# Kernel optimization log

Measured on AMD Instinct MI355X. Metric: run time of the kernel, lower is better.

Reference implementation:

```python
import jax, jax.numpy as jnp
import numpy as np

B, T, C, H = 2, 2048, 1024, 16
HD = C // H
HID = C * 4 // 3  # 1365, SwiGLU hidden
EPS = 1e-5


def _ln(x, g, b):
    m = x.mean(-1, keepdims=True)
    v = ((x - m) ** 2).mean(-1, keepdims=True)
    return (x - m) / jnp.sqrt(v + EPS) * g + b


def setup_inputs() -> dict:
    key0 = jax.random.key(0)
    ks = jax.random.split(key0, 16)
    s = 0.02
    inp = {
        'query': jax.random.normal(ks[0], (B, T, C), jnp.float32),
        'key': jax.random.normal(ks[1], (B, T, C), jnp.float32),
        'g_q': jnp.ones((C,), jnp.float32), 'b_q': jnp.zeros((C,), jnp.float32),
        'g_k': jnp.ones((C,), jnp.float32), 'b_k': jnp.zeros((C,), jnp.float32),
        'in_proj_w': jax.random.normal(ks[2], (3 * C, C), jnp.float32) * s,
        'in_proj_b': jnp.zeros((3 * C,), jnp.float32),
        'out_w': jax.random.normal(ks[3], (C, C), jnp.float32) * s,
        'out_b': jnp.zeros((C,), jnp.float32),
        'proj_w': jax.random.normal(ks[4], (C, C), jnp.float32) * s,
        'proj_b': jnp.zeros((C,), jnp.float32),
        'rel_table': jax.random.normal(ks[5], (H, 2 * 2048 - 1), jnp.float32) * s,
        'g_ffn': jnp.ones((C,), jnp.float32), 'b_ffn': jnp.zeros((C,), jnp.float32),
        'w1': jax.random.normal(ks[6], (HID, C), jnp.float32) * s,
        'w2': jax.random.normal(ks[7], (HID, C), jnp.float32) * s,
        'w3': jax.random.normal(ks[8], (C, HID), jnp.float32) * s,
        'g_out': jnp.ones((C,), jnp.float32), 'b_out': jnp.zeros((C,), jnp.float32),
        'max_len': 2048,
    }
    return inp


def reference(query, key, g_q, b_q, g_k, b_k, in_proj_w, in_proj_b, out_w, out_b,
              proj_w, proj_b, rel_table, g_ffn, b_ffn, w1, w2, w3, g_out, b_out, max_len):
    Tq, Tk = query.shape[1], key.shape[1]
    q = _ln(query, g_q, b_q)
    k = _ln(key, g_k, b_k)
    # in-projection (torch MHA packed weights)
    wq, wk, wv = jnp.split(in_proj_w, 3, axis=0)
    bq, bk, bv = jnp.split(in_proj_b, 3, axis=0)
    qp = (q @ wq.T + bq).reshape(B, Tq, H, HD).transpose(0, 2, 1, 3)
    kp = (k @ wk.T + bk).reshape(B, Tk, H, HD).transpose(0, 2, 1, 3)
    vp = (k @ wv.T + bv).reshape(B, Tk, H, HD).transpose(0, 2, 1, 3)
    # relative-position bias, mean over heads -> [Tq,Tk] additive mask
    rel_idx = jnp.clip(jnp.arange(Tq)[:, None] - jnp.arange(Tk)[None, :] + (max_len - 1),
                       0, 2 * max_len - 2)
    mask = rel_table[:, rel_idx].mean(axis=0)  # [Tq,Tk]
    scores = jnp.einsum('bhqd,bhkd->bhqk', qp, kp) / jnp.sqrt(jnp.float32(HD))
    attn = jax.nn.softmax(scores + mask[None, None], axis=-1)
    ctx = jnp.einsum('bhqk,bhkd->bhqd', attn, vp)
    ctx = ctx.transpose(0, 2, 1, 3).reshape(B, Tq, C)
    attn_out = ctx @ out_w.T + out_b
    attn_out = attn_out @ proj_w.T + proj_b
    x = query + attn_out
    # SwiGLU FFN (proj dropout/dropout are identity at eval)
    h = _ln(x, g_ffn, b_ffn)
    ff = (jax.nn.silu(h @ w1.T) * (h @ w2.T)) @ w3.T
    x = x + ff
    return _ln(x, g_out, b_out)
```

## Files before the change

kernel.cpp:

```cpp
#include <hip/hip_runtime.h>
#include <hip/hip_bf16.h>

static constexpr int Bb  = 2;
static constexpr int Tt  = 2048;
static constexpr int Cc  = 1024;
static constexpr int Hh  = 16;
static constexpr int HDi = 64;
static constexpr int HID = 1365;
static constexpr int HIDP = 1408;
static constexpr int Mm  = Bb * Tt;

typedef unsigned short u16;
typedef __attribute__((ext_vector_type(8))) short bf16x8;
typedef __attribute__((ext_vector_type(4))) float f32x4;
typedef __attribute__((ext_vector_type(8))) unsigned short u16x8;
typedef __attribute__((ext_vector_type(4))) unsigned short u16x4;

__device__ inline u16 f2bf(float f) {
    unsigned u = __builtin_bit_cast(unsigned, f);
    u += 0x7fffu + ((u >> 16) & 1u);
    return (u16)(u >> 16);
}

__device__ inline unsigned cvtpk(float lo, float hi) {
    unsigned r;
    asm("v_cvt_pk_bf16_f32 %0, %1, %2" : "=v"(r) : "v"(lo), "v"(hi));
    return r;
}

__device__ inline float vexp2(float x) {
    float r;
    asm("v_exp_f32 %0, %1" : "=v"(r) : "v"(x));
    return r;
}

__device__ inline void gl16(const void* g, void* l) {
    __builtin_amdgcn_global_load_lds(
        (const __attribute__((address_space(1))) unsigned*)g,
        (__attribute__((address_space(3))) unsigned*)l, 16, 0, 0);
}

template<int OUTBF>
__global__ __launch_bounds__(256) void ln_k(const float* __restrict__ x,
                                            const float* __restrict__ g,
                                            const float* __restrict__ b,
                                            void* __restrict__ yv) {
    int row = blockIdx.x;
    int tid = threadIdx.x;
    const float4* xr = (const float4*)(x + (size_t)row * Cc);
    float4 v = xr[tid];
    float s  = v.x + v.y + v.z + v.w;
    float ss = v.x*v.x + v.y*v.y + v.z*v.z + v.w*v.w;
    __shared__ float rs[256], rq[256];
    rs[tid] = s; rq[tid] = ss;
    __syncthreads();
    for (int o = 128; o > 0; o >>= 1) {
        if (tid < o) { rs[tid] += rs[tid+o]; rq[tid] += rq[tid+o]; }
        __syncthreads();
    }
    float mean = rs[0] * (1.f/Cc);
    float var  = rq[0] * (1.f/Cc) - mean*mean;
    float inv  = rsqrtf(var + 1e-5f);
    float4 gv = ((const float4*)g)[tid];
    float4 bv = ((const float4*)b)[tid];
    float o0 = (v.x-mean)*inv*gv.x + bv.x;
    float o1 = (v.y-mean)*inv*gv.y + bv.y;
    float o2 = (v.z-mean)*inv*gv.z + bv.z;
    float o3 = (v.w-mean)*inv*gv.w + bv.w;
    if (OUTBF) {
        u16x4 o4 = { f2bf(o0), f2bf(o1), f2bf(o2), f2bf(o3) };
        ((u16x4*)((u16*)yv + (size_t)row * Cc))[tid] = o4;
    } else {
        float4 o4 = { o0, o1, o2, o3 };
        ((float4*)((float*)yv + (size_t)row * Cc))[tid] = o4;
    }
}

__global__ __launch_bounds__(256) void ln2_k(const float* __restrict__ q,
                                             const float* __restrict__ k,
                                             const float* __restrict__ gq, const float* __restrict__ bq,
                                             const float* __restrict__ gk, const float* __restrict__ bk,
                                             u16* __restrict__ qn, u16* __restrict__ kn) {
    int row = blockIdx.x;
    const float* x; const float* g; const float* bb; u16* y; int r;
    if (row < Mm) { x = q; g = gq; bb = bq; y = qn; r = row; }
    else          { x = k; g = gk; bb = bk; y = kn; r = row - Mm; }
    int tid = threadIdx.x;
    float4 v = ((const float4*)(x + (size_t)r * Cc))[tid];
    float s  = v.x + v.y + v.z + v.w;
    float ss = v.x*v.x + v.y*v.y + v.z*v.z + v.w*v.w;
    __shared__ float rs[256], rq2[256];
    rs[tid] = s; rq2[tid] = ss;
    __syncthreads();
    for (int o = 128; o > 0; o >>= 1) {
        if (tid < o) { rs[tid] += rs[tid+o]; rq2[tid] += rq2[tid+o]; }
        __syncthreads();
    }
    float mean = rs[0] * (1.f/Cc);
    float var  = rq2[0] * (1.f/Cc) - mean*mean;
    float inv  = rsqrtf(var + 1e-5f);
    float4 gv = ((const float4*)g)[tid];
    float4 bv = ((const float4*)bb)[tid];
    u16x4 o4 = { f2bf((v.x-mean)*inv*gv.x + bv.x), f2bf((v.y-mean)*inv*gv.y + bv.y),
                 f2bf((v.z-mean)*inv*gv.z + bv.z), f2bf((v.w-mean)*inv*gv.w + bv.w) };
    ((u16x4*)(y + (size_t)r * Cc))[tid] = o4;
}

__global__ __launch_bounds__(256) void prep_k(const float* __restrict__ in_proj_w, u16* __restrict__ wA,
                                              const float* __restrict__ proj_w,  u16* __restrict__ wPb,
                                              const float* __restrict__ w1, u16* __restrict__ w1b,
                                              const float* __restrict__ w2, u16* __restrict__ w2b,
                                              const float* __restrict__ w3, u16* __restrict__ w3b,
                                              const float* __restrict__ out_w, u16* __restrict__ wOt,
                                              const float* __restrict__ out_b, const float* __restrict__ bp,
                                              float* __restrict__ bc,
                                              const float* __restrict__ rel, float* __restrict__ mr) {
    __shared__ float sh[64*65];
    int bid = blockIdx.x, tid = threadIdx.x;
    if (bid < 3456) {
        int u = bid * 256 + tid;
        const float* src; u16* dst; int valid;
        if (u < 1536*256)                   { src = in_proj_w; dst = wA;  valid = 3*Cc*Cc; }
        else if ((u -= 1536*256) < 512*256) { src = proj_w;    dst = wPb; valid = Cc*Cc; }
        else if ((u -= 512*256) < 704*256)  { src = w1;        dst = w1b; valid = HID*Cc; }
        else     { u -= 704*256;              src = w2;        dst = w2b; valid = HID*Cc; }
        int e0 = u * 8;
        u16x8 o;
        if (e0 + 8 <= valid) {
            float4 a = *(const float4*)(src + e0);
            float4 b = *(const float4*)(src + e0 + 4);
            o[0]=f2bf(a.x); o[1]=f2bf(a.y); o[2]=f2bf(a.z); o[3]=f2bf(a.w);
            o[4]=f2bf(b.x); o[5]=f2bf(b.y); o[6]=f2bf(b.z); o[7]=f2bf(b.w);
        } else {
            #pragma unroll
            for (int j = 0; j < 8; j++) { int e = e0 + j; o[j] = f2bf(e < valid ? src[e] : 0.f); }
        }
        *(u16x8*)(dst + (size_t)e0) = o;
    } else if (bid < 4160) {
        int idx = (bid - 3456) * 256 + tid;
        int e0 = idx * 8;
        int r = e0 / HIDP, c0 = e0 - r * HIDP;
        u16x8 o;
        #pragma unroll
        for (int j = 0; j < 8; j++) {
            int c = c0 + j;
            o[j] = f2bf(c < HID ? w3[(size_t)r * HID + c] : 0.f);
        }
        *(u16x8*)(w3b + (size_t)e0) = o;
    } else if (bid < 4416) {
        int id = bid - 4160;
        int j0 = (id & 15) * 64, c0 = (id >> 4) * 64;
        #pragma unroll
        for (int i = 0; i < 16; i++) {
            int e = tid + i*256;
            int c = e >> 6, j = e & 63;
            sh[c*65 + j] = out_w[(size_t)(c0 + c) * Cc + j0 + j];
        }
        __syncthreads();
        #pragma unroll
        for (int i = 0; i < 16; i++) {
            int e = tid + i*256;
            int j = e >> 6, c = e & 63;
            wOt[(size_t)(j0 + j) * Cc + c0 + c] = f2bf(sh[c*65 + j]);
        }
    } else if (bid < 5440) {
        int i = bid - 4416;
        float4 w = ((const float4*)(proj_w + (size_t)i * Cc))[tid];
        float4 b = ((const float4*)out_b)[tid];
        float s = w.x*b.x + w.y*b.y + w.z*b.z + w.w*b.w;
        sh[tid] = s; __syncthreads();
        for (int o = 128; o > 0; o >>= 1) {
            if (tid < o) sh[tid] += sh[tid+o];
            __syncthreads();
        }
        if (tid == 0) bc[i] = sh[0] + bp[i];
    } else {
        int j = (bid - 5440) * 256 + tid;
        if (j < 2*Tt - 1) {
            float s = 0.f;
            #pragma unroll
            for (int h = 0; h < Hh; h++) s += rel[(size_t)h * (2*Tt - 1) + j];
            mr[j] = s * (1.f/Hh);
        }
    }
}

template<int OUTBF, int HASRES, int HASBIAS>
__global__ __launch_bounds__(256) void mgemm64_k(const u16* __restrict__ A,
                                                 const u16* __restrict__ W,
                                                 const float* __restrict__ bias,
                                                 const float* __restrict__ res,
                                                 void* __restrict__ outv,
                                                 int N, int K) {
    __shared__ u16 As[2][64*32];
    __shared__ u16 Ws[2][128*32];
    int bm = blockIdx.y * 64, bn = blockIdx.x * 128;
    int tid = threadIdx.x, w = tid >> 6, l = tid & 63;
    int lr = l & 15, lh = l >> 4;
    int wm = (w >> 1) * 32, wn = (w & 1) * 64;
    f32x4 acc[2][4] = {};

    auto stage = [&](int buf, int kt) {
        {
            int row = tid >> 2, slot = tid & 3;
            int ko = kt + ((slot ^ (row & 3)) << 3);
            gl16(A + (size_t)(bm + row) * K + ko, (char*)As[buf] + tid * 16);
        }
        #pragma unroll
        for (int c = 0; c < 2; c++) {
            int i = c*256 + tid;
            int row = i >> 2, slot = i & 3;
            int ko = kt + ((slot ^ (row & 3)) << 3);
            gl16(W + (size_t)(bn + row) * K + ko, (char*)Ws[buf] + (c*256 + tid) * 16);
        }
    };
    stage(0, 0);
    for (int kt = 0; kt < K; kt += 32) {
        int buf = (kt >> 5) & 1;
        __syncthreads();
        if (kt + 32 < K) stage(buf ^ 1, kt + 32);
        bf16x8 af[2], wf[4];
        #pragma unroll
        for (int f = 0; f < 2; f++) {
            int r = wm + f*16 + lr;
            af[f] = *(const bf16x8*)((const char*)As[buf] + r*64 + ((lh ^ (r & 3)) << 4));
        }
        #pragma unroll
        for (int f = 0; f < 4; f++) {
            int rn = wn + f*16 + lr;
            wf[f] = *(const bf16x8*)((const char*)Ws[buf] + rn*64 + ((lh ^ (rn & 3)) << 4));
        }
        #pragma unroll
        for (int fm = 0; fm < 2; fm++)
            #pragma unroll
            for (int fn = 0; fn < 4; fn++)
                acc[fm][fn] = __builtin_amdgcn_mfma_f32_16x16x32_bf16(af[fm], wf[fn], acc[fm][fn], 0, 0, 0);
    }

    #pragma unroll
    for (int fm = 0; fm < 2; fm++) {
        #pragma unroll
        for (int r = 0; r < 4; r++) {
            int row = bm + wm + fm*16 + lh*4 + r;
            #pragma unroll
            for (int fn = 0; fn < 4; fn++) {
                int col = bn + wn + fn*16 + lr;
                float v = acc[fm][fn][r];
                if (HASBIAS) v += bias[col];
                if (HASRES)  v += res[(size_t)row * N + col];
                if (OUTBF) ((u16*)outv)[(size_t)row * N + col] = f2bf(v);
                else       ((float*)outv)[(size_t)row * N + col] = v;
            }
        }
    }
}

__global__ __launch_bounds__(256) void mqkv_k(const u16* __restrict__ qn,
                                              const u16* __restrict__ kn,
                                              const u16* __restrict__ wA,
                                              const float* __restrict__ bias3,
                                              u16* __restrict__ out3,
                                              const u16* __restrict__ wPb,
                                              const u16* __restrict__ wOt,
                                              u16* __restrict__ wCb) {
    int z = blockIdx.z;
    const u16* A; const u16* W; const float* bias = bias3; u16* out;
    if (z < 3) { A = z ? kn : qn; W = wA + (size_t)z * Cc * Cc; bias = bias3 + z * Cc; out = out3 + (size_t)z * Mm * Cc; }
    else       { if (blockIdx.y >= 8) return; A = wPb; W = wOt; out = wCb; }

    __shared__ u16 As[2][128*32];
    __shared__ u16 Ws[2][128*32];
    int bm = blockIdx.y * 128, bn = blockIdx.x * 128;
    int tid = threadIdx.x, w = tid >> 6, l = tid & 63;
    int lr = l & 15, lh = l >> 4;
    int wm = (w >> 1) * 64, wn = (w & 1) * 64;
    f32x4 acc[4][4] = {};

    auto stage = [&](int buf, int kt) {
        #pragma unroll
        for (int c = 0; c < 2; c++) {
            int i = w*128 + c*64 + l;
            int row = i >> 2, slot = i & 3;
            int ko = kt + ((slot ^ (row & 3)) << 3);
            gl16(A + (size_t)(bm + row) * Cc + ko, (char*)As[buf] + (w*128 + c*64) * 16);
            gl16(W + (size_t)(bn + row) * Cc + ko, (char*)Ws[buf] + (w*128 + c*64) * 16);
        }
    };
    stage(0, 0);
    for (int kt = 0; kt < Cc; kt += 32) {
        int buf = (kt >> 5) & 1;
        __syncthreads();
        if (kt + 32 < Cc) stage(buf ^ 1, kt + 32);
        bf16x8 af[4], wf[4];
        #pragma unroll
        for (int f = 0; f < 4; f++) {
            int r = wm + f*16 + lr;
            af[f] = *(const bf16x8*)((const char*)As[buf] + r*64 + ((lh ^ (r & 3)) << 4));
            int rn = wn + f*16 + lr;
            wf[f] = *(const bf16x8*)((const char*)Ws[buf] + rn*64 + ((lh ^ (rn & 3)) << 4));
        }
        #pragma unroll
        for (int fm = 0; fm < 4; fm++)
            #pragma unroll
            for (int fn = 0; fn < 4; fn++)
                acc[fm][fn] = __builtin_amdgcn_mfma_f32_16x16x32_bf16(af[fm], wf[fn], acc[fm][fn], 0, 0, 0);
    }

    #pragma unroll
    for (int fm = 0; fm < 4; fm++) {
        #pragma unroll
        for (int r = 0; r < 4; r++) {
            int row = bm + wm + fm*16 + lh*4 + r;
            #pragma unroll
            for (int fn = 0; fn < 4; fn++) {
                int col = bn + wn + fn*16 + lr;
                float v = acc[fm][fn][r];
                if (z < 3) v += bias[col];
                out[(size_t)row * Cc + col] = f2bf(v);
            }
        }
    }
}

__global__ __launch_bounds__(256) void mswiglu64_k(const u16* __restrict__ A,
                                                   const u16* __restrict__ W1,
                                                   const u16* __restrict__ W2,
                                                   u16* __restrict__ out,
                                                   int N, int K) {
    __shared__ u16 As[2][64*32];
    __shared__ u16 W1s[2][128*32];
    __shared__ u16 W2s[2][128*32];
    int bm = blockIdx.y * 64, bn = blockIdx.x * 128;
    int tid = threadIdx.x, w = tid >> 6, l = tid & 63;
    int lr = l & 15, lh = l >> 4;
    int wm = (w >> 1) * 32, wn = (w & 1) * 64;
    f32x4 acc1[2][4] = {};
    f32x4 acc2[2][4] = {};

    auto stage = [&](int buf, int kt) {
        {
            int row = tid >> 2, slot = tid & 3;
            int ko = kt + ((slot ^ (row & 3)) << 3);
            gl16(A + (size_t)(bm + row) * K + ko, (char*)As[buf] + tid * 16);
        }
        #pragma unroll
        for (int c = 0; c < 2; c++) {
            int i = c*256 + tid;
            int row = i >> 2, slot = i & 3;
            int ko = kt + ((slot ^ (row & 3)) << 3);
            gl16(W1 + (size_t)(bn + row) * K + ko, (char*)W1s[buf] + (c*256 + tid) * 16);
            gl16(W2 + (size_t)(bn + row) * K + ko, (char*)W2s[buf] + (c*256 + tid) * 16);
        }
    };
    stage(0, 0);
    for (int kt = 0; kt < K; kt += 32) {
        int buf = (kt >> 5) & 1;
        __syncthreads();
        if (kt + 32 < K) stage(buf ^ 1, kt + 32);
        bf16x8 af[2], w1f[4], w2f[4];
        #pragma unroll
        for (int f = 0; f < 2; f++) {
            int r = wm + f*16 + lr;
            af[f] = *(const bf16x8*)((const char*)As[buf] + r*64 + ((lh ^ (r & 3)) << 4));
        }
        #pragma unroll
        for (int f = 0; f < 4; f++) {
            int rn = wn + f*16 + lr;
            int offn = rn*64 + ((lh ^ (rn & 3)) << 4);
            w1f[f] = *(const bf16x8*)((const char*)W1s[buf] + offn);
            w2f[f] = *(const bf16x8*)((const char*)W2s[buf] + offn);
        }
        #pragma unroll
        for (int fm = 0; fm < 2; fm++)
            #pragma unroll
            for (int fn = 0; fn < 4; fn++) {
                acc1[fm][fn] = __builtin_amdgcn_mfma_f32_16x16x32_bf16(af[fm], w1f[fn], acc1[fm][fn], 0, 0, 0);
                acc2[fm][fn] = __builtin_amdgcn_mfma_f32_16x16x32_bf16(af[fm], w2f[fn], acc2[fm][fn], 0, 0, 0);
            }
    }

    #pragma unroll
    for (int fm = 0; fm < 2; fm++) {
        #pragma unroll
        for (int r = 0; r < 4; r++) {
            int row = bm + wm + fm*16 + lh*4 + r;
            #pragma unroll
            for (int fn = 0; fn < 4; fn++) {
                int col = bn + wn + fn*16 + lr;
                float a = acc1[fm][fn][r];
                float sig = 1.f / (1.f + __expf(-a));
                out[(size_t)row * N + col] = f2bf(a * sig * acc2[fm][fn][r]);
            }
        }
    }
}

__global__ __launch_bounds__(256) void vt_k(const u16* __restrict__ vp,
                                            u16* __restrict__ vt) {
    int blk = blockIdx.x;
    int bh = blk >> 5, kb = blk & 31;
    int b = bh >> 4, h = bh & 15;
    __shared__ u16 t[64][65];
    int tid = threadIdx.x;
    size_t bc = (size_t)b*Tt*Cc + (size_t)h*HDi;
    #pragma unroll
    for (int i = 0; i < 16; i++) {
        int e = tid + i*256;
        int k = e >> 6, d = e & 63;
        t[d][k] = vp[bc + (size_t)(kb*64 + k)*Cc + d];
    }
    __syncthreads();
    #pragma unroll
    for (int i = 0; i < 16; i++) {
        int e = tid + i*256;
        int d = e >> 6, k = e & 63;
        vt[((size_t)bh*64 + d)*Tt + kb*64 + k] = t[d][k];
    }
}

__global__ __launch_bounds__(512) void fattn_k(const u16* __restrict__ qp,
                                               const u16* __restrict__ kp,
                                               const u16* __restrict__ vt,
                                               const float* __restrict__ mr,
                                               u16* __restrict__ ctx) {
    __shared__ alignas(128) u16 Kt[2*4096];
    __shared__ alignas(128) u16 Vts[2*4096];
    __shared__ float mrw[2176];

    constexpr float C1 = 0.18033688011118324f;

    int bid = blockIdx.x;
    int blk = ((bid & 7) << 6) | (bid >> 3);
    int qt = blk & 15, h = (blk >> 4) & 15, b = blk >> 8;
    int q0 = qt * 128;
    int tid = threadIdx.x, w = tid >> 6, l = tid & 63;
    int lr = l & 15, lh = l >> 4;
    size_t bc = (size_t)b * Tt * Cc + (size_t)h * HDi;
    const u16* vtb = vt + (size_t)(b*Hh + h) * HDi * Tt;

    for (int i = tid; i < 2175; i += 512) mrw[i] = mr[q0 + i] * 8.f;

    bf16x8 qa[2];
    {
        const u16* qrow = qp + bc + (size_t)(q0 + w*16 + lr) * Cc;
        qa[0] = *(const bf16x8*)(qrow + lh*8);
        qa[1] = *(const bf16x8*)(qrow + 32 + lh*8);
    }

    f32x4 oacc[4] = {};
    float mrun = -1e30f, lrun = 0.f;

    const char* pKb0 = (const char*)Kt + (lr>>2)*1024 + (lr&3)*128
                       + ((lh ^ (lr & 3)) << 4) + (((lr >> 2) & 1) << 6);
    const char* pKb1 = (const char*)((size_t)pKb0 ^ 64);
    int g6 = ((((lr >> 2) ^ (lr >> 3)) & 1) << 6);
    const char* pV0 = (const char*)Vts + lr*128 + ((lh ^ (lr & 3)) << 4) + g6;
    const char* pV1 = (const char*)((size_t)pV0 ^ 64);
    const char* pm = (const char*)mrw + (w*16 + lr - lh*8 + 2047 - 39) * 4;

    int sl = tid & 7, kr0 = tid >> 3;
    int so = (sl ^ (kr0 & 7) ^ (((kr0 >> 3) & 1) << 2)) << 3;
    const u16* gK = kp + bc + (size_t)kr0 * Cc + so;
    const u16* gV = vtb + (size_t)kr0 * Tt + so;
    int wb = (tid & 448) * 16;
    char* dK0 = (char*)Kt  + wb;
    char* dV0 = (char*)Vts + wb;

    auto stage = [&](int bufo) {
        gl16(gK, dK0 + bufo);
        gl16(gV, dV0 + bufo);
        gK += 64*Cc;
        gV += 64;
    };

    auto tile = [&](int bufo) {
        f32x4 s[4];
        #pragma unroll
        for (int f = 0; f < 4; f++) {
            int ob = 39 - (f & 1)*32 - (f >> 1)*4;
            s[f][0] = *(const float*)(pm + (ob    ) * 4);
            s[f][1] = *(const float*)(pm + (ob - 1) * 4);
            s[f][2] = *(const float*)(pm + (ob - 2) * 4);
            s[f][3] = *(const float*)(pm + (ob - 3) * 4);
        }
        pm -= 256;
        __builtin_amdgcn_s_setprio(1);
        {
            const char* k0 = pKb0 + bufo;
            const char* k1 = pKb1 + bufo;
            bf16x8 kb;
            kb = *(const bf16x8*)(k0 + 0);    s[0] = __builtin_amdgcn_mfma_f32_16x16x32_bf16(kb, qa[0], s[0], 0, 0, 0);
            kb = *(const bf16x8*)(k1 + 0);    s[0] = __builtin_amdgcn_mfma_f32_16x16x32_bf16(kb, qa[1], s[0], 0, 0, 0);
            kb = *(const bf16x8*)(k0 + 4096); s[1] = __builtin_amdgcn_mfma_f32_16x16x32_bf16(kb, qa[0], s[1], 0, 0, 0);
            kb = *(const bf16x8*)(k1 + 4096); s[1] = __builtin_amdgcn_mfma_f32_16x16x32_bf16(kb, qa[1], s[1], 0, 0, 0);
            kb = *(const bf16x8*)(k1 + 512);  s[2] = __builtin_amdgcn_mfma_f32_16x16x32_bf16(kb, qa[0], s[2], 0, 0, 0);
            kb = *(const bf16x8*)(k0 + 512);  s[2] = __builtin_amdgcn_mfma_f32_16x16x32_bf16(kb, qa[1], s[2], 0, 0, 0);
            kb = *(const bf16x8*)(k1 + 4608); s[3] = __builtin_amdgcn_mfma_f32_16x16x32_bf16(kb, qa[0], s[3], 0, 0, 0);
            kb = *(const bf16x8*)(k0 + 4608); s[3] = __builtin_amdgcn_mfma_f32_16x16x32_bf16(kb, qa[1], s[3], 0, 0, 0);
        }
        __builtin_amdgcn_s_setprio(0);

        float tm = -1e30f;
        #pragma unroll
        for (int f = 0; f < 4; f++)
            #pragma unroll
            for (int r = 0; r < 4; r++) tm = fmaxf(tm, s[f][r]);
        tm = fmaxf(tm, __shfl_xor(tm, 16));
        tm = fmaxf(tm, __shfl_xor(tm, 32));

        float corr = 1.f;
        bool nod = __all(tm <= mrun + 64.f);
        if (!nod) {
            float mn = fmaxf(mrun, tm);
            corr = vexp2((mrun - mn) * C1);
            mrun = mn;
        }
        float mnc = mrun * C1;
        float ts = 0.f;
        #pragma unroll
        for (int f = 0; f < 4; f++)
            #pragma unroll
            for (int r = 0; r < 4; r++) {
                float e = vexp2(fmaf(s[f][r], C1, -mnc));
                s[f][r] = e; ts += e;
            }
        ts += __shfl_xor(ts, 16);
        ts += __shfl_xor(ts, 32);
        if (nod) {
            lrun += ts;
        } else {
            lrun = lrun*corr + ts;
            #pragma unroll
            for (int f = 0; f < 4; f++) {
                oacc[f][0] *= corr; oacc[f][1] *= corr;
                oacc[f][2] *= corr; oacc[f][3] *= corr;
            }
        }

        uint4 pb0u = { cvtpk(s[0][0], s[0][1]), cvtpk(s[0][2], s[0][3]),
                       cvtpk(s[2][0], s[2][1]), cvtpk(s[2][2], s[2][3]) };
        uint4 pb1u = { cvtpk(s[1][0], s[1][1]), cvtpk(s[1][2], s[1][3]),
                       cvtpk(s[3][0], s[3][1]), cvtpk(s[3][2], s[3][3]) };
        bf16x8 pb0 = __builtin_bit_cast(bf16x8, pb0u);
        bf16x8 pb1 = __builtin_bit_cast(bf16x8, pb1u);

        __builtin_amdgcn_s_setprio(1);
        #pragma unroll
        for (int f = 0; f < 4; f++) {
            bf16x8 vb0 = *(const bf16x8*)(pV0 + bufo + f*2048);
            oacc[f] = __builtin_amdgcn_mfma_f32_16x16x32_bf16(vb0, pb0, oacc[f], 0, 0, 0);
            bf16x8 vb1 = *(const bf16x8*)(pV1 + bufo + f*2048);
            oacc[f] = __builtin_amdgcn_mfma_f32_16x16x32_bf16(vb1, pb1, oacc[f], 0, 0, 0);
        }
        __builtin_amdgcn_s_setprio(0);
    };

    stage(0);
    #pragma unroll 1
    for (int kt = 0; kt < 32; kt += 2) {
        __syncthreads();
        stage(8192);
        tile(0);
        __syncthreads();
        if (kt < 30) stage(0);
        tile(8192);
    }

    float iv = 1.f / lrun;
    size_t rowoff = bc + (size_t)(q0 + w*16 + lr) * Cc;
    #pragma unroll
    for (int f = 0; f < 4; f++) {
        u16x4 o4 = { f2bf(oacc[f][0]*iv), f2bf(oacc[f][1]*iv),
                     f2bf(oacc[f][2]*iv), f2bf(oacc[f][3]*iv) };
        *(u16x4*)(ctx + rowoff + f*16 + lh*4) = o4;
    }
}

extern "C" void kernel_launch(void* const* d_in, const int* in_sizes, int n_in,
                              void* d_out, int out_size, void* d_ws, size_t ws_size,
                              hipStream_t stream) {
    const float* query     = (const float*)d_in[0];
    const float* key       = (const float*)d_in[1];
    const float* g_q       = (const float*)d_in[2];
    const float* b_q       = (const float*)d_in[3];
    const float* g_k       = (const float*)d_in[4];
    const float* b_k       = (const float*)d_in[5];
    const float* in_proj_w = (const float*)d_in[6];
    const float* in_proj_b = (const float*)d_in[7];
    const float* out_w     = (const float*)d_in[8];
    const float* out_b     = (const float*)d_in[9];
    const float* proj_w    = (const float*)d_in[10];
    const float* proj_b    = (const float*)d_in[11];
    const float* rel_table = (const float*)d_in[12];
    const float* g_ffn     = (const float*)d_in[13];
    const float* b_ffn     = (const float*)d_in[14];
    const float* w1        = (const float*)d_in[15];
    const float* w2        = (const float*)d_in[16];
    const float* w3        = (const float*)d_in[17];
    const float* g_out     = (const float*)d_in[18];
    const float* b_out     = (const float*)d_in[19];

    char* p = (char*)d_ws;
    auto alloc = [&](size_t bytes) { char* r = p; p += bytes; return r; };
    const size_t MCb = (size_t)Mm * Cc * 2;
    u16* wA  = (u16*)alloc((size_t)3*Cc*Cc*2);
    u16* wPb = (u16*)alloc((size_t)Cc*Cc*2);
    u16* wOt = (u16*)alloc((size_t)Cc*Cc*2);
    u16* wCb = (u16*)alloc((size_t)Cc*Cc*2);
    u16* w1b = (u16*)alloc((size_t)HIDP*Cc*2);
    u16* w2b = (u16*)alloc((size_t)HIDP*Cc*2);
    u16* w3b = (u16*)alloc((size_t)Cc*HIDP*2);
    float* bc = (float*)alloc(Cc*4);
    float* mr = (float*)alloc(4096*4);
    u16* qn = (u16*)alloc(MCb);
    u16* kn = (u16*)alloc(MCb);
    u16* qp = (u16*)alloc(MCb);
    u16* kp = (u16*)alloc(MCb);
    u16* vp = (u16*)alloc(MCb);
    u16* vt = (u16*)alloc(MCb);
    float* x  = (float*)alloc((size_t)Mm*Cc*4);
    float* x2 = (float*)alloc((size_t)Mm*Cc*4);
    u16* ctx = qn;
    u16* h   = qp;
    u16* gf  = vp;

    dim3 blk(256);
    prep_k<<<5456, blk, 0, stream>>>(in_proj_w, wA, proj_w, wPb, w1, w1b, w2, w2b,
                                     w3, w3b, out_w, wOt, out_b, proj_b, bc, rel_table, mr);

    ln2_k<<<2*Mm, blk, 0, stream>>>(query, key, g_q, b_q, g_k, b_k, qn, kn);

    dim3 gqkv(Cc/128, Mm/128, 4);
    mqkv_k<<<gqkv, blk, 0, stream>>>(qn, kn, wA, in_proj_b, qp, wPb, wOt, wCb);

    vt_k<<<Bb*Hh*32, blk, 0, stream>>>(vp, vt);
    fattn_k<<<Bb*Hh*16, dim3(512), 0, stream>>>(qp, kp, vt, mr, ctx);

    dim3 g1(Cc/128, Mm/64);
    mgemm64_k<0,1,1><<<g1, blk, 0, stream>>>(ctx, wCb, bc, query, x, Cc, Cc);

    ln_k<1><<<Mm, blk, 0, stream>>>(x, g_ffn, b_ffn, h);
    dim3 g2(HIDP/128, Mm/64);
    mswiglu64_k<<<g2, blk, 0, stream>>>(h, w1b, w2b, gf, HIDP, Cc);
    dim3 g3(Cc/128, Mm/64);
    mgemm64_k<0,1,0><<<g3, blk, 0, stream>>>(gf, w3b, nullptr, x, x2, Cc, HIDP);

    ln_k<0><<<Mm, blk, 0, stream>>>(x2, g_out, b_out, d_out);
}
```

Baseline: 256.9 us.

## Register-staged prefetch pipeline and XCD-aware flat grid for QKV GEMM

```diff
diff --git a/kernel.cpp b/kernel.cpp
--- a/kernel.cpp
+++ b/kernel.cpp
@@ -255,6 +255,8 @@
     }
 }
 
+struct StageRegs { uint4 a0, a1, w0, w1; };
+
 __global__ __launch_bounds__(256) void mqkv_k(const u16* __restrict__ qn,
                                               const u16* __restrict__ kn,
                                               const u16* __restrict__ wA,
@@ -263,34 +265,53 @@
                                               const u16* __restrict__ wPb,
                                               const u16* __restrict__ wOt,
                                               u16* __restrict__ wCb) {
-    int z = blockIdx.z;
-    const u16* A; const u16* W; const float* bias = bias3; u16* out;
-    if (z < 3) { A = z ? kn : qn; W = wA + (size_t)z * Cc * Cc; bias = bias3 + z * Cc; out = out3 + (size_t)z * Mm * Cc; }
-    else       { if (blockIdx.y >= 8) return; A = wPb; W = wOt; out = wCb; }
-
     __shared__ u16 As[2][128*32];
     __shared__ u16 Ws[2][128*32];
-    int bm = blockIdx.y * 128, bn = blockIdx.x * 128;
+
+    int bid = blockIdx.x;
+    int xcd = bid & 7, j = bid >> 3;
+    int p = xcd * 13 + (j >> 3), x = j & 7;
+    const u16* A; const u16* W; const float* bias = bias3; u16* out;
+    int bm, bn = x * 128, hasb;
+    if (p < 96) {
+        int z = p >> 5, y = p & 31;
+        A = z ? kn : qn; W = wA + (size_t)z * Cc * Cc;
+        bias = bias3 + z * Cc; out = out3 + (size_t)z * Mm * Cc;
+        bm = y * 128; hasb = 1;
+    } else {
+        A = wPb; W = wOt; out = wCb;
+        bm = (p - 96) * 128; hasb = 0;
+    }
+
     int tid = threadIdx.x, w = tid >> 6, l = tid & 63;
     int lr = l & 15, lh = l >> 4;
     int wm = (w >> 1) * 64, wn = (w & 1) * 64;
     f32x4 acc[4][4] = {};
 
-    auto stage = [&](int buf, int kt) {
-        #pragma unroll
-        for (int c = 0; c < 2; c++) {
-            int i = w*128 + c*64 + l;
-            int row = i >> 2, slot = i & 3;
-            int ko = kt + ((slot ^ (row & 3)) << 3);
-            gl16(A + (size_t)(bm + row) * Cc + ko, (char*)As[buf] + (w*128 + c*64) * 16);
-            gl16(W + (size_t)(bn + row) * Cc + ko, (char*)Ws[buf] + (w*128 + c*64) * 16);
-        }
+    int row = tid >> 1, half = tid & 1;
+    const u16* gA = A + (size_t)(bm + row) * Cc + half * 16;
+    const u16* gW = W + (size_t)(bn + row) * Cc + half * 16;
+    int sw0 = ((2*half)     ^ (row & 3)) << 4;
+    int sw1 = ((2*half + 1) ^ (row & 3)) << 4;
+
+    StageRegs sA, sB;
+    auto ld = [&](StageRegs& s, int t) {
+        const u16* pa = gA + t*32;
+        const u16* pw = gW + t*32;
+        s.a0 = *(const uint4*)pa;
+        s.a1 = *(const uint4*)(pa + 8);
+        s.w0 = *(const uint4*)pw;
+        s.w1 = *(const uint4*)(pw + 8);
     };
-    stage(0, 0);
-    for (int kt = 0; kt < Cc; kt += 32) {
-        int buf = (kt >> 5) & 1;
-        __syncthreads();
-        if (kt + 32 < Cc) stage(buf ^ 1, kt + 32);
+    auto st = [&](int buf, const StageRegs& s) {
+        char* ba = (char*)As[buf] + row*64;
+        char* bw = (char*)Ws[buf] + row*64;
+        *(uint4*)(ba + sw0) = s.a0;
+        *(uint4*)(ba + sw1) = s.a1;
+        *(uint4*)(bw + sw0) = s.w0;
+        *(uint4*)(bw + sw1) = s.w1;
+    };
+    auto comp = [&](int buf) {
         bf16x8 af[4], wf[4];
         #pragma unroll
         for (int f = 0; f < 4; f++) {
@@ -304,19 +325,36 @@
             #pragma unroll
             for (int fn = 0; fn < 4; fn++)
                 acc[fm][fn] = __builtin_amdgcn_mfma_f32_16x16x32_bf16(af[fm], wf[fn], acc[fm][fn], 0, 0, 0);
+    };
+
+    ld(sA, 0);
+    ld(sB, 1);
+    st(0, sA);
+    ld(sA, 2);
+    __syncthreads();
+    #pragma unroll 1
+    for (int t = 0; t < 32; t += 2) {
+        st(1, sB);
+        if (t + 3 < 32) ld(sB, t + 3);
+        comp(0);
+        __syncthreads();
+        if (t + 2 < 32) st(0, sA);
+        if (t + 4 < 32) ld(sA, t + 4);
+        comp(1);
+        __syncthreads();
     }
 
     #pragma unroll
     for (int fm = 0; fm < 4; fm++) {
         #pragma unroll
         for (int r = 0; r < 4; r++) {
-            int row = bm + wm + fm*16 + lh*4 + r;
+            int orow = bm + wm + fm*16 + lh*4 + r;
             #pragma unroll
             for (int fn = 0; fn < 4; fn++) {
                 int col = bn + wn + fn*16 + lr;
                 float v = acc[fm][fn][r];
-                if (z < 3) v += bias[col];
-                out[(size_t)row * Cc + col] = f2bf(v);
+                if (hasb) v += bias[col];
+                out[(size_t)orow * Cc + col] = f2bf(v);
             }
         }
     }
@@ -630,8 +668,7 @@
 
     ln2_k<<<2*Mm, blk, 0, stream>>>(query, key, g_q, b_q, g_k, b_k, qn, kn);
 
-    dim3 gqkv(Cc/128, Mm/128, 4);
-    mqkv_k<<<gqkv, blk, 0, stream>>>(qn, kn, wA, in_proj_b, qp, wPb, wOt, wCb);
+    mqkv_k<<<832, blk, 0, stream>>>(qn, kn, wA, in_proj_b, qp, wPb, wOt, wCb);
 
     vt_k<<<Bb*Hh*32, blk, 0, stream>>>(vp, vt);
     fattn_k<<<Bb*Hh*16, dim3(512), 0, stream>>>(qp, kp, vt, mr, ctx);
```

After: 348.7 us. 1.36x slower.

## Triple-buffer QKV GEMM with XCD-aware 1D grid and explicit waitcnt

Applied to the files above, without the earlier changes.

```diff
diff --git a/kernel.cpp b/kernel.cpp
--- a/kernel.cpp
+++ b/kernel.cpp
@@ -263,20 +263,31 @@
                                               const u16* __restrict__ wPb,
                                               const u16* __restrict__ wOt,
                                               u16* __restrict__ wCb) {
-    int z = blockIdx.z;
+    __shared__ u16 As[3][128*32];
+    __shared__ u16 Ws[3][128*32];
+
+    int bid = blockIdx.x;
+    int xcd = bid & 7, j = bid >> 3;
+    int p = xcd * 13 + (j >> 3), x = j & 7;
     const u16* A; const u16* W; const float* bias = bias3; u16* out;
-    if (z < 3) { A = z ? kn : qn; W = wA + (size_t)z * Cc * Cc; bias = bias3 + z * Cc; out = out3 + (size_t)z * Mm * Cc; }
-    else       { if (blockIdx.y >= 8) return; A = wPb; W = wOt; out = wCb; }
-
-    __shared__ u16 As[2][128*32];
-    __shared__ u16 Ws[2][128*32];
-    int bm = blockIdx.y * 128, bn = blockIdx.x * 128;
+    int bm, bn = x * 128, hasb;
+    if (p < 96) {
+        int z = p >> 5, y = p & 31;
+        A = z ? kn : qn; W = wA + (size_t)z * Cc * Cc;
+        bias = bias3 + z * Cc; out = out3 + (size_t)z * Mm * Cc;
+        bm = y * 128; hasb = 1;
+    } else {
+        A = wPb; W = wOt; out = wCb;
+        bm = (p - 96) * 128; hasb = 0;
+    }
+
     int tid = threadIdx.x, w = tid >> 6, l = tid & 63;
     int lr = l & 15, lh = l >> 4;
     int wm = (w >> 1) * 64, wn = (w & 1) * 64;
     f32x4 acc[4][4] = {};
 
-    auto stage = [&](int buf, int kt) {
+    auto stage = [&](int buf, int t) {
+        int kt = t * 32;
         #pragma unroll
         for (int c = 0; c < 2; c++) {
             int i = w*128 + c*64 + l;
@@ -286,11 +297,7 @@
             gl16(W + (size_t)(bn + row) * Cc + ko, (char*)Ws[buf] + (w*128 + c*64) * 16);
         }
     };
-    stage(0, 0);
-    for (int kt = 0; kt < Cc; kt += 32) {
-        int buf = (kt >> 5) & 1;
-        __syncthreads();
-        if (kt + 32 < Cc) stage(buf ^ 1, kt + 32);
+    auto comp = [&](int buf) {
         bf16x8 af[4], wf[4];
         #pragma unroll
         for (int f = 0; f < 4; f++) {
@@ -304,19 +311,36 @@
             #pragma unroll
             for (int fn = 0; fn < 4; fn++)
                 acc[fm][fn] = __builtin_amdgcn_mfma_f32_16x16x32_bf16(af[fm], wf[fn], acc[fm][fn], 0, 0, 0);
-    }
+    };
+
+    stage(0, 0);
+    stage(1, 1);
+    #pragma unroll 1
+    for (int t = 0; t < 31; t++) {
+        asm volatile("s_waitcnt vmcnt(4)" ::: "memory");
+        __builtin_amdgcn_sched_barrier(0);
+        __builtin_amdgcn_s_barrier();
+        if (t + 2 < 32) stage((t + 2) % 3, t + 2);
+        comp(t % 3);
+        asm volatile("s_waitcnt lgkmcnt(0)" ::: "memory");
+        __builtin_amdgcn_sched_barrier(0);
+    }
+    asm volatile("s_waitcnt vmcnt(0)" ::: "memory");
+    __builtin_amdgcn_sched_barrier(0);
+    __builtin_amdgcn_s_barrier();
+    comp(31 % 3);
 
     #pragma unroll
     for (int fm = 0; fm < 4; fm++) {
         #pragma unroll
         for (int r = 0; r < 4; r++) {
-            int row = bm + wm + fm*16 + lh*4 + r;
+            int orow = bm + wm + fm*16 + lh*4 + r;
             #pragma unroll
             for (int fn = 0; fn < 4; fn++) {
                 int col = bn + wn + fn*16 + lr;
                 float v = acc[fm][fn][r];
-                if (z < 3) v += bias[col];
-                out[(size_t)row * Cc + col] = f2bf(v);
+                if (hasb) v += bias[col];
+                out[(size_t)orow * Cc + col] = f2bf(v);
             }
         }
     }
@@ -630,8 +654,7 @@
 
     ln2_k<<<2*Mm, blk, 0, stream>>>(query, key, g_q, b_q, g_k, b_k, qn, kn);
 
-    dim3 gqkv(Cc/128, Mm/128, 4);
-    mqkv_k<<<gqkv, blk, 0, stream>>>(qn, kn, wA, in_proj_b, qp, wPb, wOt, wCb);
+    mqkv_k<<<832, blk, 0, stream>>>(qn, kn, wA, in_proj_b, qp, wPb, wOt, wCb);
 
     vt_k<<<Bb*Hh*32, blk, 0, stream>>>(vp, vt);
     fattn_k<<<Bb*Hh*16, dim3(512), 0, stream>>>(qp, kp, vt, mr, ctx);
```

After: 255.8 us. Within noise of the previous version (-0.5%).
